# Kernel tuning notes

Measured on AMD Instinct MI355X. Metric: run time of the kernel, lower is better.

## Reference

```python
import jax, jax.numpy as jnp
import numpy as np

HIDDEN = 2048
N_HEADS = 16
N_KV = 4
HEAD_DIM = 128
EPS = 1e-6
B, S = 2, 2048


def rms_norm(x, w, eps=EPS):
    xf = x.astype(jnp.float32)
    var = jnp.mean(xf * xf, axis=-1, keepdims=True)
    return (w * (xf * jax.lax.rsqrt(var + eps))).astype(x.dtype)


def rotate_half(x):
    half = x.shape[-1] // 2
    return jnp.concatenate([-x[..., half:], x[..., :half]], axis=-1)


def setup_inputs() -> dict:
    key = jax.random.key(0)
    ks = jax.random.split(key, 9)
    inv_freq = 1.0 / (10000.0 ** (np.arange(0, HEAD_DIM, 2) / HEAD_DIM))
    ang = np.arange(S)[:, None] * inv_freq[None, :]
    ang = np.concatenate([ang, ang], axis=-1)  # [S, HEAD_DIM]
    return {
        "hidden_states": jax.random.normal(ks[0], (B, S, HIDDEN), jnp.float32),
        "cos": jnp.asarray(np.cos(ang), jnp.float32),
        "sin": jnp.asarray(np.sin(ang), jnp.float32),
        "Wq": jax.random.normal(ks[1], (HIDDEN, N_HEADS * HEAD_DIM), jnp.float32) * 0.02,
        "Wk": jax.random.normal(ks[2], (HIDDEN, N_KV * HEAD_DIM), jnp.float32) * 0.02,
        "Wv": jax.random.normal(ks[3], (HIDDEN, N_KV * HEAD_DIM), jnp.float32) * 0.02,
        "Wo": jax.random.normal(ks[4], (N_HEADS * HEAD_DIM, HIDDEN), jnp.float32) * 0.02,
        "q_norm_w": jnp.ones((HEAD_DIM,), jnp.float32),
        "k_norm_w": jnp.ones((HEAD_DIM,), jnp.float32),
    }


def reference(hidden_states, cos, sin, Wq, Wk, Wv, Wo, q_norm_w, k_norm_w):
    b, s, _ = hidden_states.shape
    n_rep = N_HEADS // N_KV
    scaling = HEAD_DIM ** -0.5

    q = (hidden_states @ Wq).reshape(b, s, N_HEADS, HEAD_DIM)
    k = (hidden_states @ Wk).reshape(b, s, N_KV, HEAD_DIM)
    v = (hidden_states @ Wv).reshape(b, s, N_KV, HEAD_DIM)

    q = rms_norm(q, q_norm_w)
    k = rms_norm(k, k_norm_w)

    q = q.transpose(0, 2, 1, 3)  # [b, h, s, d]
    k = k.transpose(0, 2, 1, 3)  # [b, kv, s, d]
    v = v.transpose(0, 2, 1, 3)

    c = cos[None, None]  # [1,1,s,d]
    si = sin[None, None]
    q = q * c + rotate_half(q) * si
    k = k * c + rotate_half(k) * si

    # repeat kv heads to match query heads
    k = jnp.repeat(k, n_rep, axis=1)
    v = jnp.repeat(v, n_rep, axis=1)

    scores = jnp.einsum("bhqd,bhkd->bhqk", q, k) * scaling
    causal = jnp.triu(jnp.full((s, s), -jnp.inf, jnp.float32), k=1)
    scores = scores + causal
    attn = jax.nn.softmax(scores.astype(jnp.float32), axis=-1).astype(q.dtype)

    out = jnp.einsum("bhqk,bhkd->bhqd", attn, v)
    out = out.transpose(0, 2, 1, 3).reshape(b, s, N_HEADS * HEAD_DIM)
    return out @ Wo
```

## Files before the change

kernel.cpp:

```cpp
#include <hip/hip_runtime.h>

typedef float floatx4 __attribute__((ext_vector_type(4)));
typedef short short8 __attribute__((ext_vector_type(8)));

#define HIDDEN 2048
#define NH 16
#define NKV 4
#define HD 128
#define NB 2
#define SEQ 2048
#define MT (NB * SEQ)
#define NQKV 3072

#define MFMA16(a, b, c) __builtin_amdgcn_mfma_f32_16x16x32_bf16(a, b, c, 0, 0, 0)
#define S_BAR() __builtin_amdgcn_s_barrier()
#define WAIT_LGKM0() do { asm volatile("s_waitcnt lgkmcnt(0)" ::: "memory"); \
                          __builtin_amdgcn_sched_barrier(0); } while (0)
#define WAIT_VM(N) do { asm volatile("s_waitcnt vmcnt(" #N ")" ::: "memory"); \
                        __builtin_amdgcn_sched_barrier(0); } while (0)

__device__ __forceinline__ unsigned short f2bf(float x) {
  union { float f; unsigned u; } v; v.f = x;
  unsigned r = v.u + 0x7FFFu + ((v.u >> 16) & 1u);
  return (unsigned short)(r >> 16);
}

__device__ __forceinline__ unsigned int cvt_pk_bf16(float lo, float hi) {
  unsigned int r;
  asm("v_cvt_pk_bf16_f32 %0, %1, %2" : "=v"(r) : "v"(lo), "v"(hi));
  return r;
}

__global__ void cast_bf16_kernel(const float* __restrict__ in,
                                 unsigned short* __restrict__ out, int n4) {
  int i = blockIdx.x * 256 + threadIdx.x;
  if (i >= n4) return;
  float4 v = ((const float4*)in)[i];
  ushort4 o;
  o.x = f2bf(v.x); o.y = f2bf(v.y); o.z = f2bf(v.z); o.w = f2bf(v.w);
  ((ushort4*)out)[i] = o;
}

__global__ void wtrans_kernel(const float* __restrict__ Wq,
                              const float* __restrict__ Wk,
                              const float* __restrict__ Wv,
                              const float* __restrict__ Wo,
                              unsigned short* __restrict__ wqkvt,
                              unsigned short* __restrict__ wot) {
  __shared__ float tile[32][33];
  int z = blockIdx.z;
  int nt = blockIdx.x * 32;
  int k0 = blockIdx.y * 32;
  const float* src;
  unsigned short* dst;
  int Nd, scol0, drow0;
  if (z == 0) {
    src = Wq; Nd = 2048; scol0 = nt; drow0 = nt; dst = wqkvt;
  } else if (z == 1) {
    src = Wo; Nd = 2048; scol0 = nt; drow0 = nt; dst = wot;
  } else {
    if (nt >= 1024) return;
    Nd = 512; dst = wqkvt; drow0 = 2048 + nt;
    if (nt < 512) { src = Wk; scol0 = nt; }
    else          { src = Wv; scol0 = nt - 512; }
  }
  int tx = threadIdx.x, ty = threadIdx.y;
  for (int i = 0; i < 32; i += 8)
    tile[ty + i][tx] = src[(size_t)(k0 + ty + i) * Nd + scol0 + tx];
  __syncthreads();
  for (int i = 0; i < 32; i += 8)
    dst[(size_t)(drow0 + ty + i) * HIDDEN + k0 + tx] = f2bf(tile[tx][ty + i]);
}


__global__ __launch_bounds__(512, 1)
void gemm_qkv_kernel(const unsigned short* __restrict__ A,
                     const unsigned short* __restrict__ Bt,
                     const float* __restrict__ qw,
                     const float* __restrict__ kw,
                     const float* __restrict__ cosb,
                     const float* __restrict__ sinb,
                     unsigned short* __restrict__ Qb,
                     unsigned short* __restrict__ Kbb,
                     unsigned short* __restrict__ Vt) {
  extern __shared__ __align__(16) char smem[];
  const int tid = threadIdx.x;
  const int wave = tid >> 6, lane = tid & 63;
  const int quad = lane >> 4, l16 = lane & 15;
  const int m0 = blockIdx.x * 256, n0 = blockIdx.y * 256;
  const int wm = (wave >> 2) * 128, wn = (wave & 3) * 64;

  const int sgrow = wave * 8 + (lane >> 3);
  const int swzcol = (((lane & 7) ^ ((lane >> 3) & 7)) << 4);
  const int laneA0 = l16 * 128 + ((quad ^ (l16 & 7)) << 4);
  const int laneA1 = laneA0 ^ 64;

  auto stageA = [&](int T, int h) {
    const char* g = (const char*)A + (((size_t)(m0 + h * 128)) * HIDDEN + T * 64) * 2;
    char* l = smem + (size_t)(((T & 1) * 2 + h) * 16384) + wave * 1024;
#pragma unroll
    for (int ii = 0; ii < 2; ++ii) {
      const char* src = g + (size_t)(ii * 64 + sgrow) * (HIDDEN * 2) + swzcol;
      __builtin_amdgcn_global_load_lds(
          (const __attribute__((address_space(1))) unsigned int*)src,
          (__attribute__((address_space(3))) unsigned int*)(l + ii * 8192), 16, 0, 0);
    }
  };
  auto stageB = [&](int T, int h) {
    const char* g = (const char*)Bt + (((size_t)(n0 + h * 128)) * HIDDEN + T * 64) * 2;
    char* l = smem + 65536 + (size_t)(((T & 1) * 2 + h) * 16384) + wave * 1024;
#pragma unroll
    for (int ii = 0; ii < 2; ++ii) {
      const char* src = g + (size_t)(ii * 64 + sgrow) * (HIDDEN * 2) + swzcol;
      __builtin_amdgcn_global_load_lds(
          (const __attribute__((address_space(1))) unsigned int*)src,
          (__attribute__((address_space(3))) unsigned int*)(l + ii * 8192), 16, 0, 0);
    }
  };

  floatx4 acc[8][4] = {};
  short8 a[4][2], bA[2][2], bB[2][2];
  const int NT = HIDDEN / 64;

  stageA(0, 0); stageA(0, 1); stageB(0, 0); stageB(0, 1);
  stageB(1, 0); stageB(1, 1);
  WAIT_VM(4);
  S_BAR();

#pragma unroll 1
  for (int Y = 0; Y < NT; ++Y) {
    const int cb = Y & 1;
    const char* Ah = smem + (size_t)((cb * 2 + (wave >> 2)) * 16384);
    const char* Bh = smem + 65536 + (size_t)((cb * 2 + ((wave & 3) >> 1)) * 16384) +
                     (wn & 64) * 128;
    if (Y + 1 < NT) stageA(Y + 1, 0);
#pragma unroll
    for (int fi = 0; fi < 4; ++fi) {
      a[fi][0] = *(const short8*)(Ah + fi * 2048 + laneA0);
      a[fi][1] = *(const short8*)(Ah + fi * 2048 + laneA1);
    }
#pragma unroll
    for (int fj = 0; fj < 2; ++fj) {
      bA[fj][0] = *(const short8*)(Bh + fj * 2048 + laneA0);
      bA[fj][1] = *(const short8*)(Bh + fj * 2048 + laneA1);
    }
    WAIT_LGKM0();
    __builtin_amdgcn_s_setprio(1);
#pragma unroll
    for (int fi = 0; fi < 4; ++fi)
#pragma unroll
      for (int fj = 0; fj < 2; ++fj) {
        acc[fi][fj] = MFMA16(a[fi][0], bA[fj][0], acc[fi][fj]);
        acc[fi][fj] = MFMA16(a[fi][1], bA[fj][1], acc[fi][fj]);
      }
    __builtin_amdgcn_s_setprio(0);
    S_BAR();
    if (Y + 1 < NT) stageA(Y + 1, 1);
#pragma unroll
    for (int fj = 0; fj < 2; ++fj) {
      bB[fj][0] = *(const short8*)(Bh + 4096 + fj * 2048 + laneA0);
      bB[fj][1] = *(const short8*)(Bh + 4096 + fj * 2048 + laneA1);
    }
    WAIT_LGKM0();
    __builtin_amdgcn_s_setprio(1);
#pragma unroll
    for (int fi = 0; fi < 4; ++fi)
#pragma unroll
      for (int fj = 0; fj < 2; ++fj) {
        acc[fi][2 + fj] = MFMA16(a[fi][0], bB[fj][0], acc[fi][2 + fj]);
        acc[fi][2 + fj] = MFMA16(a[fi][1], bB[fj][1], acc[fi][2 + fj]);
      }
    __builtin_amdgcn_s_setprio(0);
    S_BAR();
    if (Y + 2 < NT) stageB(Y + 2, 0);
#pragma unroll
    for (int fi = 0; fi < 4; ++fi) {
      a[fi][0] = *(const short8*)(Ah + 8192 + fi * 2048 + laneA0);
      a[fi][1] = *(const short8*)(Ah + 8192 + fi * 2048 + laneA1);
    }
    WAIT_LGKM0();
    __builtin_amdgcn_s_setprio(1);
#pragma unroll
    for (int fi = 0; fi < 4; ++fi)
#pragma unroll
      for (int fj = 0; fj < 2; ++fj) {
        acc[4 + fi][2 + fj] = MFMA16(a[fi][0], bB[fj][0], acc[4 + fi][2 + fj]);
        acc[4 + fi][2 + fj] = MFMA16(a[fi][1], bB[fj][1], acc[4 + fi][2 + fj]);
      }
    __builtin_amdgcn_s_setprio(0);
    S_BAR();
    if (Y + 2 < NT) stageB(Y + 2, 1);
    __builtin_amdgcn_s_setprio(1);
#pragma unroll
    for (int fi = 0; fi < 4; ++fi)
#pragma unroll
      for (int fj = 0; fj < 2; ++fj) {
        acc[4 + fi][fj] = MFMA16(a[fi][0], bA[fj][0], acc[4 + fi][fj]);
        acc[4 + fi][fj] = MFMA16(a[fi][1], bA[fj][1], acc[4 + fi][fj]);
      }
    __builtin_amdgcn_s_setprio(0);
    if (Y + 2 < NT) { WAIT_VM(4); } else { WAIT_VM(0); }
    S_BAR();
  }

  const int tileN = blockIdx.y;
  const int head2 = tileN * 2 + ((wave & 3) >> 1);

  if (tileN >= 10) {
    const int kv = head2 - (NH + NKV);
#pragma unroll
    for (int i = 0; i < 8; ++i) {
      int m = m0 + wm + (i >> 2) * 64 + (i & 3) * 16 + quad * 4;
      int b = m >> 11, sbase = m & (SEQ - 1);
#pragma unroll
      for (int j = 0; j < 4; ++j) {
        int d = (wave & 1) * 64 + (j >> 1) * 32 + (j & 1) * 16 + l16;
        ushort4 pk;
        pk.x = f2bf(acc[i][j][0]); pk.y = f2bf(acc[i][j][1]);
        pk.z = f2bf(acc[i][j][2]); pk.w = f2bf(acc[i][j][3]);
        *(ushort4*)&Vt[((size_t)(b * NKV + kv) * HD + d) * SEQ + sbase] = pk;
      }
    }
    return;
  }

  float* pscr = (float*)smem;
  float* pssq = (float*)(smem + 8 * 64 * 20 * 4);
  const float* w = (head2 < NH) ? qw : kw;
  float wown[4], wpar[4];
#pragma unroll
  for (int j = 0; j < 4; ++j) {
    int d = (wave & 1) * 64 + (j >> 1) * 32 + (j & 1) * 16 + l16;
    wown[j] = w[d];
    wpar[j] = w[d ^ 64];
  }
#pragma unroll 1
  for (int i = 0; i < 8; ++i) {
    float sq[4];
#pragma unroll
    for (int r = 0; r < 4; ++r) {
      float s2 = acc[i][0][r] * acc[i][0][r] + acc[i][1][r] * acc[i][1][r] +
                 acc[i][2][r] * acc[i][2][r] + acc[i][3][r] * acc[i][3][r];
#pragma unroll
      for (int off = 1; off < 16; off <<= 1) s2 += __shfl_xor(s2, off, 64);
      sq[r] = s2;
    }
    if (l16 == 0)
      *(float4*)&pssq[wave * 16 + quad * 4] = make_float4(sq[0], sq[1], sq[2], sq[3]);
#pragma unroll
    for (int j = 0; j < 4; ++j)
      *(float4*)&pscr[(wave * 64 + j * 16 + l16) * 20 + quad * 4] = *(float4*)&acc[i][j];
    __syncthreads();
    float4 oss = *(const float4*)&pssq[(wave ^ 1) * 16 + quad * 4];
    float rr[4];
    rr[0] = rsqrtf((sq[0] + oss.x) * (1.0f / 128.0f) + 1e-6f);
    rr[1] = rsqrtf((sq[1] + oss.y) * (1.0f / 128.0f) + 1e-6f);
    rr[2] = rsqrtf((sq[2] + oss.z) * (1.0f / 128.0f) + 1e-6f);
    rr[3] = rsqrtf((sq[3] + oss.w) * (1.0f / 128.0f) + 1e-6f);
    int mbase = m0 + wm + (i >> 2) * 64 + (i & 3) * 16 + quad * 4;
    int b = mbase >> 11, sbase = mbase & (SEQ - 1);
#pragma unroll
    for (int j = 0; j < 4; ++j) {
      float4 par = *(const float4*)&pscr[((wave ^ 1) * 64 + j * 16 + l16) * 20 + quad * 4];
      float pr[4] = {par.x, par.y, par.z, par.w};
      int d = (wave & 1) * 64 + (j >> 1) * 32 + (j & 1) * 16 + l16;
      unsigned short* dst = (head2 < NH)
          ? Qb + ((size_t)(b * NH + head2) * SEQ + sbase) * HD + d
          : Kbb + ((size_t)(b * NKV + (head2 - NH)) * SEQ + sbase) * HD + d;
#pragma unroll
      for (int r = 0; r < 4; ++r) {
        int s = sbase + r;
        float c = cosb[s * HD + d], sn = sinb[s * HD + d];
        float xo = acc[i][j][r] * rr[r] * wown[j];
        float xp = pr[r] * rr[r] * wpar[j];
        float out = ((wave & 1) == 0) ? (xo * c - xp * sn) : (xo * c + xp * sn);
        dst[(size_t)r * HD] = f2bf(out);
      }
    }
    __syncthreads();
  }
}

__global__ __launch_bounds__(512, 1)
void gemm_o_kernel(const unsigned short* __restrict__ A,
                   const unsigned short* __restrict__ Bt,
                   float* __restrict__ C) {
  extern __shared__ __align__(16) char smem[];
  const int tid = threadIdx.x;
  const int wave = tid >> 6, lane = tid & 63;
  const int quad = lane >> 4, l16 = lane & 15;
  const int m0 = blockIdx.x * 256, n0 = blockIdx.y * 128;
  const int wm = (wave >> 2) * 128, wn = (wave & 3) * 32;

  const int sgrow = wave * 8 + (lane >> 3);
  const int swzcol = (((lane & 7) ^ ((lane >> 3) & 7)) << 4);
  const int laneA0 = l16 * 128 + ((quad ^ (l16 & 7)) << 4);
  const int laneA1 = laneA0 ^ 64;

  auto stageA = [&](int T, int h) {
    const char* g = (const char*)A + (((size_t)(m0 + h * 128)) * HIDDEN + T * 64) * 2;
    char* l = smem + (size_t)(((T & 1) * 2 + h) * 16384) + wave * 1024;
#pragma unroll
    for (int ii = 0; ii < 2; ++ii) {
      const char* src = g + (size_t)(ii * 64 + sgrow) * (HIDDEN * 2) + swzcol;
      __builtin_amdgcn_global_load_lds(
          (const __attribute__((address_space(1))) unsigned int*)src,
          (__attribute__((address_space(3))) unsigned int*)(l + ii * 8192), 16, 0, 0);
    }
  };
  auto stageB = [&](int T, int h) {
    const char* g = (const char*)Bt + (((size_t)(n0 + h * 64)) * HIDDEN + T * 64) * 2;
    char* l = smem + 65536 + (size_t)(((T & 1) * 2 + h) * 8192) + wave * 1024;
    const char* src = g + (size_t)sgrow * (HIDDEN * 2) + swzcol;
    __builtin_amdgcn_global_load_lds(
        (const __attribute__((address_space(1))) unsigned int*)src,
        (__attribute__((address_space(3))) unsigned int*)l, 16, 0, 0);
  };

  floatx4 acc[8][2] = {};
  short8 a[4][2], bAv[2], bBv[2];
  const int NT = HIDDEN / 64;

  stageA(0, 0); stageA(0, 1); stageB(0, 0); stageB(0, 1);
  stageB(1, 0); stageB(1, 1);
  WAIT_VM(2);
  S_BAR();

#pragma unroll 1
  for (int Y = 0; Y < NT; ++Y) {
    const int cb = Y & 1;
    const char* Ah = smem + (size_t)((cb * 2 + (wave >> 2)) * 16384);
    const char* Bh = smem + 65536 + (size_t)((cb * 2 + ((wave & 3) >> 1)) * 8192) +
                     (wn & 32) * 128;
    if (Y + 1 < NT) stageA(Y + 1, 0);
#pragma unroll
    for (int fi = 0; fi < 4; ++fi) {
      a[fi][0] = *(const short8*)(Ah + fi * 2048 + laneA0);
      a[fi][1] = *(const short8*)(Ah + fi * 2048 + laneA1);
    }
    bAv[0] = *(const short8*)(Bh + laneA0);
    bAv[1] = *(const short8*)(Bh + laneA1);
    WAIT_LGKM0();
    __builtin_amdgcn_s_setprio(1);
#pragma unroll
    for (int fi = 0; fi < 4; ++fi) {
      acc[fi][0] = MFMA16(a[fi][0], bAv[0], acc[fi][0]);
      acc[fi][0] = MFMA16(a[fi][1], bAv[1], acc[fi][0]);
    }
    __builtin_amdgcn_s_setprio(0);
    S_BAR();
    if (Y + 1 < NT) stageA(Y + 1, 1);
    bBv[0] = *(const short8*)(Bh + 2048 + laneA0);
    bBv[1] = *(const short8*)(Bh + 2048 + laneA1);
    WAIT_LGKM0();
    __builtin_amdgcn_s_setprio(1);
#pragma unroll
    for (int fi = 0; fi < 4; ++fi) {
      acc[fi][1] = MFMA16(a[fi][0], bBv[0], acc[fi][1]);
      acc[fi][1] = MFMA16(a[fi][1], bBv[1], acc[fi][1]);
    }
    __builtin_amdgcn_s_setprio(0);
    S_BAR();
    if (Y + 2 < NT) stageB(Y + 2, 0);
#pragma unroll
    for (int fi = 0; fi < 4; ++fi) {
      a[fi][0] = *(const short8*)(Ah + 8192 + fi * 2048 + laneA0);
      a[fi][1] = *(const short8*)(Ah + 8192 + fi * 2048 + laneA1);
    }
    WAIT_LGKM0();
    __builtin_amdgcn_s_setprio(1);
#pragma unroll
    for (int fi = 0; fi < 4; ++fi) {
      acc[4 + fi][1] = MFMA16(a[fi][0], bBv[0], acc[4 + fi][1]);
      acc[4 + fi][1] = MFMA16(a[fi][1], bBv[1], acc[4 + fi][1]);
    }
    __builtin_amdgcn_s_setprio(0);
    S_BAR();
    if (Y + 2 < NT) stageB(Y + 2, 1);
    __builtin_amdgcn_s_setprio(1);
#pragma unroll
    for (int fi = 0; fi < 4; ++fi) {
      acc[4 + fi][0] = MFMA16(a[fi][0], bAv[0], acc[4 + fi][0]);
      acc[4 + fi][0] = MFMA16(a[fi][1], bAv[1], acc[4 + fi][0]);
    }
    __builtin_amdgcn_s_setprio(0);
    if (Y + 2 < NT) { WAIT_VM(2); } else { WAIT_VM(0); }
    S_BAR();
  }

#pragma unroll
  for (int i = 0; i < 8; ++i) {
    int row = m0 + wm + (i >> 2) * 64 + (i & 3) * 16 + quad * 4;
#pragma unroll
    for (int j = 0; j < 2; ++j) {
      int col = n0 + wn + j * 16 + l16;
#pragma unroll
      for (int r = 0; r < 4; ++r)
        C[(size_t)(row + r) * 2048 + col] = acc[i][j][r];
    }
  }
}

__device__ __forceinline__ void stage_rows(const unsigned short* gbase, int rowstride,
                                           unsigned short* lds, int wave, int quad,
                                           int s_cx, int s_hb) {
#pragma unroll
  for (int i = 0; i < 8; ++i) {
    const int row = i * 16 + wave * 4 + quad;
    const int sck = s_cx ^ (((2 * i + s_hb) & 3) << 2);
    __builtin_amdgcn_global_load_lds(
        (const __attribute__((address_space(1))) unsigned int*)(gbase + (size_t)row * rowstride + sck * 8),
        (__attribute__((address_space(3))) unsigned int*)(lds + (i * 4 + wave) * 512),
        16, 0, 0);
  }
}

__global__ __launch_bounds__(256, 2)
void attn_kernel(const unsigned short* __restrict__ Q,
                 const unsigned short* __restrict__ Kb,
                 const unsigned short* __restrict__ Vt,
                 unsigned short* __restrict__ O) {
  __shared__ __align__(16) unsigned short KVs[2][128 * 128];
  const int tid = threadIdx.x;
  const int wave = tid >> 6, lane = tid & 63;
  const int quad = lane >> 4, l16 = lane & 15;
  const int l3 = l16 & 3, s3 = l16 >> 3, s2 = (l16 >> 2) & 1;
  const int bh = blockIdx.x & 31;
  const int pr = blockIdx.x >> 5;
  const int b = bh >> 4, h = bh & 15, kvh = h >> 2;

  const int s_cx = (lane & 15) ^ quad;
  const int s_hb = wave >> 1;
  const int krbase = 16 * s3 + 8 * s2 + l3;
  const int f_k = l3 | ((2 * s3 + s2) << 2);
  const int kvqb = 16 * (quad >> 1) + 8 * (quad & 1);
  const int qsw = (lane & 48) | (quad << 2);
  const float CS = 0.08838834764831845f;

  const unsigned short* Kg0 = Kb + (size_t)((b * NKV + kvh) * SEQ) * HD;
  const unsigned short* Vg0 = Vt + (size_t)((b * NKV + kvh) * HD) * SEQ;

  int p = 0;
#pragma unroll 1
  for (int seg = 0; seg < 2; ++seg) {
    const int qt = seg ? pr : (31 - pr);
    const int q0 = qt * 64;
    const int nkt = (qt >> 1) + 1;
    const int qglob = q0 + wave * 16 + l16;

    const unsigned short* Qg = Q + (size_t)((b * NH + h) * SEQ + q0) * HD;
    short8 qf[4];
#pragma unroll
    for (int ks = 0; ks < 4; ++ks)
      qf[ks] = *(const short8*)&Qg[(size_t)(wave * 16 + l16) * HD + ks * 32 + quad * 8];

    floatx4 oacc[8] = {};
    float mrow = -1e30f, lrow = 0.f;

    stage_rows(Kg0, 128, KVs[p], wave, quad, s_cx, s_hb);
    __syncthreads();

    for (int kt = 0; kt < nkt; ++kt) {
      const unsigned short* KVp = KVs[p];
      floatx4 sc[8] = {};
#pragma unroll
      for (int ks = 0; ks < 4; ++ks) {
        const int cko = ((ks * 4 + quad) ^ f_k) * 8;
#pragma unroll
        for (int j = 0; j < 8; ++j) {
          const short8 kf = *(const short8*)&KVp[(krbase + 32 * (j >> 1) + 4 * (j & 1)) * 128 + cko];
          sc[j] = __builtin_amdgcn_mfma_f32_16x16x32_bf16(kf, qf[ks], sc[j], 0, 0, 0);
        }
      }
      __syncthreads();
      stage_rows(Vg0 + kt * 128, SEQ, KVs[p], wave, quad, s_cx, s_hb);
      if (kt + 1 < nkt)
        stage_rows(Kg0 + (size_t)(kt + 1) * 128 * HD, 128, KVs[p ^ 1], wave, quad, s_cx, s_hb);

      if (kt == nkt - 1) {
#pragma unroll
        for (int j = 0; j < 8; ++j) {
          const int kvj = kt * 128 + 32 * (j >> 1) + 4 * (j & 1) + kvqb;
#pragma unroll
          for (int r = 0; r < 4; ++r)
            if (kvj + r > qglob) sc[j][r] = -1e30f;
        }
      }
      float mx = -1e30f;
#pragma unroll
      for (int j = 0; j < 8; ++j)
        mx = fmaxf(mx, fmaxf(fmaxf(sc[j][0], sc[j][1]), fmaxf(sc[j][2], sc[j][3])));
      mx = fmaxf(mx, __shfl_xor(mx, 16, 64));
      mx = fmaxf(mx, __shfl_xor(mx, 32, 64));
      if (!__all(mx <= mrow + 62.0f)) {
        const float mnew = fmaxf(mrow, mx);
        const float al = __expf((mrow - mnew) * CS);
        mrow = mnew;
        lrow *= al;
#pragma unroll
        for (int r = 0; r < 4; ++r) {
          const float ar = __shfl(al, qsw + r, 64);
#pragma unroll
          for (int t = 0; t < 8; ++t) oacc[t][r] *= ar;
        }
      }
      const float mc = mrow * CS;
      float rs = 0.f;
#pragma unroll
      for (int j = 0; j < 8; ++j)
#pragma unroll
        for (int r = 0; r < 4; ++r) {
          const float pe = __expf(sc[j][r] * CS - mc);
          sc[j][r] = pe;
          rs += pe;
        }
      rs += __shfl_xor(rs, 16, 64);
      rs += __shfl_xor(rs, 32, 64);
      lrow += rs;

      unsigned int pk[8][2];
#pragma unroll
      for (int j = 0; j < 8; ++j) {
        pk[j][0] = cvt_pk_bf16(sc[j][0], sc[j][1]);
        pk[j][1] = cvt_pk_bf16(sc[j][2], sc[j][3]);
      }
      __syncthreads();
#pragma unroll
      for (int ks = 0; ks < 4; ++ks) {
        union { unsigned int u[4]; short8 s; } au;
        au.u[0] = pk[2 * ks][0];     au.u[1] = pk[2 * ks][1];
        au.u[2] = pk[2 * ks + 1][0]; au.u[3] = pk[2 * ks + 1][1];
#pragma unroll
        for (int t = 0; t < 8; ++t) {
          const int fv = l3 | (((2 * t + s3) & 3) << 2);
          const short8 vf = *(const short8*)&KVp[(t * 16 + l16) * 128 + (((ks * 4 + quad) ^ fv) * 8)];
          oacc[t] = __builtin_amdgcn_mfma_f32_16x16x32_bf16(au.s, vf, oacc[t], 0, 0, 0);
        }
      }
      p ^= 1;
    }
    float li[4];
#pragma unroll
    for (int r = 0; r < 4; ++r) li[r] = 1.0f / __shfl(lrow, qsw + r, 64);
#pragma unroll
    for (int t = 0; t < 8; ++t) {
      const int col = h * HD + t * 16 + l16;
#pragma unroll
      for (int r = 0; r < 4; ++r) {
        const int row = q0 + wave * 16 + quad * 4 + r;
        O[(size_t)(b * SEQ + row) * (NH * HD) + col] = f2bf(oacc[t][r] * li[r]);
      }
    }
  }
}

extern "C" void kernel_launch(void* const* d_in, const int* in_sizes, int n_in,
                              void* d_out, int out_size, void* d_ws, size_t ws_size,
                              hipStream_t stream) {
  const float* hidden = (const float*)d_in[0];
  const float* cosb   = (const float*)d_in[1];
  const float* sinb   = (const float*)d_in[2];
  const float* Wq     = (const float*)d_in[3];
  const float* Wk     = (const float*)d_in[4];
  const float* Wv     = (const float*)d_in[5];
  const float* Wo     = (const float*)d_in[6];
  const float* qw     = (const float*)d_in[7];
  const float* kw     = (const float*)d_in[8];
  (void)in_sizes; (void)n_in; (void)out_size; (void)ws_size;

  char* ws = (char*)d_ws;
  size_t off = 0;
  auto alloc = [&](size_t n) { char* p = ws + off; off += (n + 255) & ~(size_t)255; return p; };

  unsigned short* hb    = (unsigned short*)alloc((size_t)MT * HIDDEN * 2);
  unsigned short* wqkvt = (unsigned short*)alloc((size_t)NQKV * HIDDEN * 2);
  unsigned short* wot   = (unsigned short*)alloc((size_t)2048 * 2048 * 2);
  unsigned short* Qb  = (unsigned short*)alloc((size_t)MT * 2048 * 2);
  unsigned short* Kbb = (unsigned short*)alloc((size_t)MT * 512 * 2);
  unsigned short* Vtb = (unsigned short*)alloc((size_t)MT * 512 * 2);
  unsigned short* Ob  = (unsigned short*)alloc((size_t)MT * 2048 * 2);

  static bool attr_done = false;
  if (!attr_done) {
    hipFuncSetAttribute((const void*)gemm_qkv_kernel,
                        hipFuncAttributeMaxDynamicSharedMemorySize, 131072);
    hipFuncSetAttribute((const void*)gemm_o_kernel,
                        hipFuncAttributeMaxDynamicSharedMemorySize, 98304);
    attr_done = true;
  }

  cast_bf16_kernel<<<(MT * HIDDEN / 4) / 256, 256, 0, stream>>>(hidden, hb, MT * HIDDEN / 4);
  dim3 tb(32, 8);
  wtrans_kernel<<<dim3(64, 64, 3), tb, 0, stream>>>(Wq, Wk, Wv, Wo, wqkvt, wot);

  gemm_qkv_kernel<<<dim3(MT / 256, NQKV / 256), 512, 131072, stream>>>(
      hb, wqkvt, qw, kw, cosb, sinb, Qb, Kbb, Vtb);

  attn_kernel<<<512, 256, 0, stream>>>(Qb, Kbb, Vtb, Ob);

  gemm_o_kernel<<<dim3(MT / 256, 2048 / 128), 512, 98304, stream>>>(Ob, wot, (float*)d_out);
}
```

Baseline: 333.5 us.

## Prefetch A two tiles ahead and remap workgroups for XCD-aware L2 locality

```diff
diff --git a/kernel.cpp b/kernel.cpp
--- a/kernel.cpp
+++ b/kernel.cpp
@@ -16,8 +16,8 @@
 #define S_BAR() __builtin_amdgcn_s_barrier()
 #define WAIT_LGKM0() do { asm volatile("s_waitcnt lgkmcnt(0)" ::: "memory"); \
                           __builtin_amdgcn_sched_barrier(0); } while (0)
-#define WAIT_VM(N) do { asm volatile("s_waitcnt vmcnt(" #N ")" ::: "memory"); \
-                        __builtin_amdgcn_sched_barrier(0); } while (0)
+#define WAIT_VM(N) asm volatile("s_waitcnt vmcnt(" #N ")" ::: "memory")
+#define LGKM_HINT8() asm volatile("s_waitcnt lgkmcnt(8)" ::: "memory")
 
 __device__ __forceinline__ unsigned short f2bf(float x) {
   union { float f; unsigned u; } v; v.f = x;
@@ -87,7 +87,11 @@
   const int tid = threadIdx.x;
   const int wave = tid >> 6, lane = tid & 63;
   const int quad = lane >> 4, l16 = lane & 15;
-  const int m0 = blockIdx.x * 256, n0 = blockIdx.y * 256;
+  const int nwg = gridDim.x * gridDim.y;
+  const int orig = blockIdx.x + gridDim.x * blockIdx.y;
+  const int lin = (orig & 7) * (nwg >> 3) + (orig >> 3);
+  const int bx = lin % gridDim.x, by = lin / gridDim.x;
+  const int m0 = bx * 256, n0 = by * 256;
   const int wm = (wave >> 2) * 128, wn = (wave & 3) * 64;
 
   const int sgrow = wave * 8 + (lane >> 3);
@@ -123,8 +127,8 @@
   const int NT = HIDDEN / 64;
 
   stageA(0, 0); stageA(0, 1); stageB(0, 0); stageB(0, 1);
-  stageB(1, 0); stageB(1, 1);
-  WAIT_VM(4);
+  stageA(1, 0); stageA(1, 1); stageB(1, 0); stageB(1, 1);
+  WAIT_VM(8);
   S_BAR();
 
 #pragma unroll 1
@@ -133,7 +137,6 @@
     const char* Ah = smem + (size_t)((cb * 2 + (wave >> 2)) * 16384);
     const char* Bh = smem + 65536 + (size_t)((cb * 2 + ((wave & 3) >> 1)) * 16384) +
                      (wn & 64) * 128;
-    if (Y + 1 < NT) stageA(Y + 1, 0);
 #pragma unroll
     for (int fi = 0; fi < 4; ++fi) {
       a[fi][0] = *(const short8*)(Ah + fi * 2048 + laneA0);
@@ -144,6 +147,8 @@
       bA[fj][0] = *(const short8*)(Bh + fj * 2048 + laneA0);
       bA[fj][1] = *(const short8*)(Bh + fj * 2048 + laneA1);
     }
+    LGKM_HINT8();
+    S_BAR();
     WAIT_LGKM0();
     __builtin_amdgcn_s_setprio(1);
 #pragma unroll
@@ -155,12 +160,12 @@
       }
     __builtin_amdgcn_s_setprio(0);
     S_BAR();
-    if (Y + 1 < NT) stageA(Y + 1, 1);
 #pragma unroll
     for (int fj = 0; fj < 2; ++fj) {
       bB[fj][0] = *(const short8*)(Bh + 4096 + fj * 2048 + laneA0);
       bB[fj][1] = *(const short8*)(Bh + 4096 + fj * 2048 + laneA1);
     }
+    S_BAR();
     WAIT_LGKM0();
     __builtin_amdgcn_s_setprio(1);
 #pragma unroll
@@ -172,12 +177,13 @@
       }
     __builtin_amdgcn_s_setprio(0);
     S_BAR();
-    if (Y + 2 < NT) stageB(Y + 2, 0);
 #pragma unroll
     for (int fi = 0; fi < 4; ++fi) {
       a[fi][0] = *(const short8*)(Ah + 8192 + fi * 2048 + laneA0);
       a[fi][1] = *(const short8*)(Ah + 8192 + fi * 2048 + laneA1);
     }
+    if (Y + 2 < NT) { stageB(Y + 2, 0); stageB(Y + 2, 1); }
+    S_BAR();
     WAIT_LGKM0();
     __builtin_amdgcn_s_setprio(1);
 #pragma unroll
@@ -189,7 +195,8 @@
       }
     __builtin_amdgcn_s_setprio(0);
     S_BAR();
-    if (Y + 2 < NT) stageB(Y + 2, 1);
+    if (Y + 2 < NT) { stageA(Y + 2, 0); stageA(Y + 2, 1); }
+    S_BAR();
     __builtin_amdgcn_s_setprio(1);
 #pragma unroll
     for (int fi = 0; fi < 4; ++fi)
@@ -199,11 +206,11 @@
         acc[4 + fi][fj] = MFMA16(a[fi][1], bA[fj][1], acc[4 + fi][fj]);
       }
     __builtin_amdgcn_s_setprio(0);
-    if (Y + 2 < NT) { WAIT_VM(4); } else { WAIT_VM(0); }
-    S_BAR();
-  }
-
-  const int tileN = blockIdx.y;
+    if (Y + 2 < NT) { WAIT_VM(8); } else { WAIT_VM(0); }
+    S_BAR();
+  }
+
+  const int tileN = by;
   const int head2 = tileN * 2 + ((wave & 3) >> 1);
 
   if (tileN >= 10) {
@@ -289,7 +296,11 @@
   const int tid = threadIdx.x;
   const int wave = tid >> 6, lane = tid & 63;
   const int quad = lane >> 4, l16 = lane & 15;
-  const int m0 = blockIdx.x * 256, n0 = blockIdx.y * 128;
+  const int nwg = gridDim.x * gridDim.y;
+  const int orig = blockIdx.x + gridDim.x * blockIdx.y;
+  const int lin = (orig & 7) * (nwg >> 3) + (orig >> 3);
+  const int bx = lin % gridDim.x, by = lin / gridDim.x;
+  const int m0 = bx * 256, n0 = by * 128;
   const int wm = (wave >> 2) * 128, wn = (wave & 3) * 32;
 
   const int sgrow = wave * 8 + (lane >> 3);
@@ -322,8 +333,8 @@
   const int NT = HIDDEN / 64;
 
   stageA(0, 0); stageA(0, 1); stageB(0, 0); stageB(0, 1);
-  stageB(1, 0); stageB(1, 1);
-  WAIT_VM(2);
+  stageA(1, 0); stageA(1, 1); stageB(1, 0); stageB(1, 1);
+  WAIT_VM(6);
   S_BAR();
 
 #pragma unroll 1
@@ -332,7 +343,6 @@
     const char* Ah = smem + (size_t)((cb * 2 + (wave >> 2)) * 16384);
     const char* Bh = smem + 65536 + (size_t)((cb * 2 + ((wave & 3) >> 1)) * 8192) +
                      (wn & 32) * 128;
-    if (Y + 1 < NT) stageA(Y + 1, 0);
 #pragma unroll
     for (int fi = 0; fi < 4; ++fi) {
       a[fi][0] = *(const short8*)(Ah + fi * 2048 + laneA0);
@@ -340,6 +350,8 @@
     }
     bAv[0] = *(const short8*)(Bh + laneA0);
     bAv[1] = *(const short8*)(Bh + laneA1);
+    LGKM_HINT8();
+    S_BAR();
     WAIT_LGKM0();
     __builtin_amdgcn_s_setprio(1);
 #pragma unroll
@@ -349,9 +361,9 @@
     }
     __builtin_amdgcn_s_setprio(0);
     S_BAR();
-    if (Y + 1 < NT) stageA(Y + 1, 1);
     bBv[0] = *(const short8*)(Bh + 2048 + laneA0);
     bBv[1] = *(const short8*)(Bh + 2048 + laneA1);
+    S_BAR();
     WAIT_LGKM0();
     __builtin_amdgcn_s_setprio(1);
 #pragma unroll
@@ -361,12 +373,13 @@
     }
     __builtin_amdgcn_s_setprio(0);
     S_BAR();
-    if (Y + 2 < NT) stageB(Y + 2, 0);
 #pragma unroll
     for (int fi = 0; fi < 4; ++fi) {
       a[fi][0] = *(const short8*)(Ah + 8192 + fi * 2048 + laneA0);
       a[fi][1] = *(const short8*)(Ah + 8192 + fi * 2048 + laneA1);
     }
+    if (Y + 2 < NT) { stageB(Y + 2, 0); stageB(Y + 2, 1); }
+    S_BAR();
     WAIT_LGKM0();
     __builtin_amdgcn_s_setprio(1);
 #pragma unroll
@@ -376,7 +389,8 @@
     }
     __builtin_amdgcn_s_setprio(0);
     S_BAR();
-    if (Y + 2 < NT) stageB(Y + 2, 1);
+    if (Y + 2 < NT) { stageA(Y + 2, 0); stageA(Y + 2, 1); }
+    S_BAR();
     __builtin_amdgcn_s_setprio(1);
 #pragma unroll
     for (int fi = 0; fi < 4; ++fi) {
@@ -384,7 +398,7 @@
       acc[4 + fi][0] = MFMA16(a[fi][1], bAv[1], acc[4 + fi][0]);
     }
     __builtin_amdgcn_s_setprio(0);
-    if (Y + 2 < NT) { WAIT_VM(2); } else { WAIT_VM(0); }
+    if (Y + 2 < NT) { WAIT_VM(6); } else { WAIT_VM(0); }
     S_BAR();
   }
 
```

Measured after the change: 346.6 us. 3.9% more time.
